# Kernel tuning notes

Measured on AMD Instinct MI355X. Metric: run time of the kernel, lower is better.

Reference implementation:

```python
import jax, jax.numpy as jnp
import numpy as np

B, L, DIM, H, DQK, DV = 4, 512, 1024, 8, 64, 64
ANGLE_BASE = 1.0 / 1024.0
EPS = 1e-5


def _xavier(key, out_d, in_d, gain):
    bound = gain * np.sqrt(6.0 / (in_d + out_d))
    return jax.random.uniform(key, (out_d, in_d), jnp.float32, -bound, bound)


def setup_inputs():
    key = jax.random.key(0)
    ks = jax.random.split(key, 9)
    # p_angle buffer: angle_base ** linspace(0,1,H*DQK) reshaped to [H, DQK]
    p_angle = (ANGLE_BASE ** jnp.linspace(0.0, 1.0, H * DQK)).reshape(H, DQK)
    return {
        "x": jax.random.normal(ks[0], (B, L, DIM), jnp.float32),
        "hidden": 0.1 * jax.random.normal(ks[1], (B, H, DQK, DV, 2), jnp.float32),
        "w_qk": _xavier(ks[2], H * DQK * 4, DIM, 0.01), "b_qk": jnp.zeros((H * DQK * 4,), jnp.float32),
        "w_v": _xavier(ks[3], H * DV * 2, DIM, 0.01), "b_v": jnp.zeros((H * DV * 2,), jnp.float32),
        "w_g": _xavier(ks[4], H * DV * 2, DIM, 0.01), "b_g": jnp.zeros((H * DV * 2,), jnp.float32),
        "w_a": _xavier(ks[5], H, DIM, 1e-4), "b_a": jnp.zeros((H,), jnp.float32),
        "w_y": _xavier(ks[6], DIM, H * DV * 2, 0.01), "b_y": jnp.zeros((DIM,), jnp.float32),
        "gn_w": jnp.ones((H,), jnp.float32), "gn_b": jnp.zeros((H,), jnp.float32),
        "p_angle": p_angle,
    }


def _sioconv(x, hidden, w_qk, b_qk, w_v, b_v, w_g, b_g, w_a, b_a, w_y, b_y, gn_w, gn_b, p_angle):
    b, l = x.shape[0], x.shape[1]
    hid = hidden[..., 0] + 1j * hidden[..., 1]                       # [B,H,I,V] complex
    v_r = (x @ w_v.T + b_v).reshape(b, l, H, DV, 2)
    v = v_r[..., 0] + 1j * v_r[..., 1]                                # [B,L,H,V]
    qk_r = (x @ w_qk.T + b_qk).reshape(b, l, H, DQK, 2, 2)
    qk = qk_r[..., 0] + 1j * qk_r[..., 1]                             # [B,L,H,I,2]
    q, k = qk[..., 0], qk[..., 1]
    a_angle = x @ w_a.T + b_a                                         # [B,L,H]
    ln_a = (1j * a_angle - 1.0) * p_angle[:, 0]                       # [B,L,H] complex
    t = jnp.arange(l, dtype=jnp.float32)
    ppq = jnp.exp(1j * (t[:, None, None] * p_angle[None]))            # [L,H,I] = exp(+i*angle*l)
    qp = q * ppq[None]
    kp = k * jnp.conj(ppq)[None]                                      # exp(-i*angle*l)
    # Decay matrix. The FFT conv with ones computes a causal prefix sum, so
    # c[b,h,l,m] = exp(sum_{j=m+1..l} ln_a[b,j,h]) for m<=l, else 0.
    S = jnp.cumsum(ln_a, axis=1)                                      # [B,L,H]
    Sh = jnp.transpose(S, (0, 2, 1))                                  # [B,H,L]
    mask = jnp.tril(jnp.ones((l, l), bool))
    diff = jnp.where(mask, Sh[:, :, :, None] - Sh[:, :, None, :], 0.0)
    c = jnp.where(mask, jnp.exp(diff), 0.0)                           # [B,H,L,L]
    qck = jnp.einsum('blhi,bmhi->bhlm', qp, kp) * c
    h_inner = jnp.einsum('bhlm,bmhv->blhv', qck, v)
    d = jnp.exp(S)                                                    # [B,L,H] cumulative decay
    p1 = jnp.exp(1j * p_angle)                                        # [H,I]
    h_cross = jnp.einsum('blhi,bhiv->blhv', qp * d[..., None], hid * p1[None, :, :, None])
    h = h_inner + h_cross                                             # [B,L,H,V]
    pp_inv = jnp.exp(1j * ((l - 1.0 - t)[:, None, None] * p_angle[None]))  # [L,H,I]
    hid_next = jnp.einsum('blhi,bhl,lhi,blhv->bhiv', k, c[:, :, -1, :], pp_inv, v)
    hid_next = hid_next + jnp.exp(S[:, -1, :])[:, :, None, None] * hid * jnp.exp(1j * p_angle * l)[None, :, :, None]
    # GroupNorm(num_head, num_head) on real view [B*L, H, V, 2]: normalize over (V,2) per head.
    hr = jnp.stack([h.real, h.imag], axis=-1)                         # [B,L,H,V,2]
    mu = hr.mean(axis=(3, 4), keepdims=True)
    var = hr.var(axis=(3, 4), keepdims=True)
    hn = (hr - mu) / jnp.sqrt(var + EPS)
    hn = hn * gn_w[None, None, :, None, None] + gn_b[None, None, :, None, None]
    h_flat = hn.reshape(b, l, H * DV * 2)
    g = x @ w_g.T + b_g
    y = (h_flat * (g * jax.nn.sigmoid(g))) @ w_y.T + b_y
    return y, hid_next


def reference(x, hidden, w_qk, b_qk, w_v, b_v, w_g, b_g, w_a, b_a, w_y, b_y, gn_w, gn_b, p_angle):
    return _sioconv(x, hidden, w_qk, b_qk, w_v, b_v, w_g, b_g, w_a, b_a, w_y, b_y, gn_w, gn_b, p_angle)
```

## Files before the change

kernel.cpp:

```cpp
#include <hip/hip_runtime.h>
#include <cstdint>
#include <cstddef>

#define B_   4
#define L_   512
#define DIM_ 1024
#define H_   8
#define DQK_ 64
#define DV_  64
#define M_   (B_ * L_)
#define EPS_ 1e-5f

typedef __attribute__((ext_vector_type(8))) short short8;
typedef __attribute__((ext_vector_type(4))) float f32x4;

__device__ __forceinline__ unsigned short f2bf(float f) {
    uint32_t u = __float_as_uint(f);
    u += 0x7FFFu + ((u >> 16) & 1u);
    return (unsigned short)(u >> 16);
}
__device__ __forceinline__ float bf2f(unsigned short u) {
    return __uint_as_float((uint32_t)u << 16);
}

__device__ __forceinline__ f32x4 mm16(short8 a, short8 b, f32x4 c) {
    return __builtin_amdgcn_mfma_f32_16x16x32_bf16(a, b, c, 0, 0, 0);
}

__device__ __forceinline__ int swoff(int r, int kb) {
    return r * 128 + (kb ^ ((r & 7) << 4));
}
__device__ __forceinline__ short8 frag(const unsigned short* p, int strip, int ks, int lane) {
    const int fr = lane & 15, fq = lane >> 4;
    const int r = strip * 16 + fr;
    return *(const short8*)((const char*)p + swoff(r, ks * 64 + fq * 16));
}

__global__ __launch_bounds__(256) void cast_all(
    const float* __restrict__ x, const float* __restrict__ wqk,
    const float* __restrict__ wv, const float* __restrict__ wg,
    const float* __restrict__ wy, const float* __restrict__ wa,
    const float* __restrict__ ba,
    unsigned short* __restrict__ xb, unsigned short* __restrict__ wall,
    unsigned short* __restrict__ wyb, float* __restrict__ babias)
{
    const int blk = blockIdx.x;
    if (blk == 7176) {
        if (threadIdx.x < 128)
            babias[threadIdx.x] = (threadIdx.x < 8) ? ba[threadIdx.x] : 0.f;
        return;
    }
    const float* src; unsigned short* dst; int base;
    if      (blk < 2048) { src = x;   dst = xb;                  base = blk; }
    else if (blk < 4096) { src = wqk; dst = wall;                base = blk - 2048; }
    else if (blk < 5120) { src = wv;  dst = wall + 2048 * 1024;  base = blk - 4096; }
    else if (blk < 6144) { src = wg;  dst = wall + 3072 * 1024;  base = blk - 5120; }
    else if (blk < 7168) { src = wy;  dst = wyb;                 base = blk - 6144; }
    else                 { src = wa;  dst = wall + 4096 * 1024;  base = blk - 7168; }
    const int i = base * 256 + threadIdx.x;
    const float4 v = ((const float4*)src)[i];
    ushort4 o;
    o.x = f2bf(v.x); o.y = f2bf(v.y); o.z = f2bf(v.z); o.w = f2bf(v.w);
    ((ushort4*)dst)[i] = o;
}

__device__ __forceinline__ void gload16(const void* g, void* l) {
    __builtin_amdgcn_global_load_lds(
        (const __attribute__((address_space(1))) unsigned int*)g,
        (__attribute__((address_space(3))) unsigned int*)l, 16, 0, 0);
}

__global__ __launch_bounds__(512) void gemm_proj(
    const unsigned short* __restrict__ A, const unsigned short* __restrict__ W,
    const float* __restrict__ bias0, const float* __restrict__ bias1,
    const float* __restrict__ bias2, const float* __restrict__ bias3,
    void* __restrict__ C0, void* __restrict__ C1,
    void* __restrict__ C2, void* __restrict__ C3,
    int n1, int n2, int n3,
    int ld0, int ld1, int ld2, int ld3,
    int bf0, int bf1, int bf2, int bf3,
    int M, int N, int K)
{
    __shared__ unsigned short sA[128 * 32];
    __shared__ unsigned short sB[128 * 32];

    const int t    = threadIdx.x;
    const int lane = t & 63;
    const int wv   = t >> 6;
    const int bm   = blockIdx.y * 128;
    const int bn   = blockIdx.x * 128;
    const int wr   = wv >> 2;
    const int wc   = wv & 3;
    const int fr   = lane & 15;
    const int fq   = lane >> 4;
    const int srow = lane >> 2;
    const int ske  = (lane & 3) * 8;

    f32x4 acc[4][2] = {};

    for (int k0 = 0; k0 < K; k0 += 32) {
        gload16(A + (size_t)(bm + wv * 16 + srow) * K + k0 + ske,
                (char*)sA + wv * 1024);
        gload16(W + (size_t)(bn + wv * 16 + srow) * K + k0 + ske,
                (char*)sB + wv * 1024);
        __syncthreads();

        short8 af[4], bf[2];
#pragma unroll
        for (int mi = 0; mi < 4; ++mi)
            af[mi] = *(const short8*)&sA[(wr * 64 + mi * 16 + fr) * 32 + fq * 8];
#pragma unroll
        for (int ni = 0; ni < 2; ++ni)
            bf[ni] = *(const short8*)&sB[(wc * 32 + ni * 16 + fr) * 32 + fq * 8];
#pragma unroll
        for (int mi = 0; mi < 4; ++mi)
#pragma unroll
            for (int ni = 0; ni < 2; ++ni)
                acc[mi][ni] = mm16(af[mi], bf[ni], acc[mi][ni]);
        __syncthreads();
    }

    void* Cb; const float* bb; int coff, ldc, isbf;
    if      (bn < n1) { Cb = C0; bb = bias0; coff = 0;  ldc = ld0; isbf = bf0; }
    else if (bn < n2) { Cb = C1; bb = bias1; coff = n1; ldc = ld1; isbf = bf1; }
    else if (bn < n3) { Cb = C2; bb = bias2; coff = n2; ldc = ld2; isbf = bf2; }
    else              { Cb = C3; bb = bias3; coff = n3; ldc = ld3; isbf = bf3; }

#pragma unroll
    for (int mi = 0; mi < 4; ++mi)
#pragma unroll
        for (int ni = 0; ni < 2; ++ni) {
            const int col = bn + wc * 32 + ni * 16 + fr - coff;
            const float bv = bb[col];
#pragma unroll
            for (int r = 0; r < 4; ++r) {
                const int row = bm + wr * 64 + mi * 16 + fq * 4 + r;
                const float val = acc[mi][ni][r] + bv;
                if (isbf)
                    ((unsigned short*)Cb)[(size_t)row * ldc + col] = f2bf(val);
                else
                    ((float*)Cb)[(size_t)row * ldc + col] = val;
            }
        }
}

__global__ __launch_bounds__(256) void gemm_y(
    const unsigned short* __restrict__ A, const unsigned short* __restrict__ W,
    const float* __restrict__ bias, float* __restrict__ C,
    int M, int N, int K)
{
    __shared__ unsigned short sA[64 * 32];
    __shared__ unsigned short sB[64 * 32];

    const int t    = threadIdx.x;
    const int lane = t & 63;
    const int wv   = t >> 6;
    const int bm   = blockIdx.y * 64;
    const int bn   = blockIdx.x * 64;
    const int wr   = wv >> 1;
    const int wc   = wv & 1;
    const int fr   = lane & 15;
    const int fq   = lane >> 4;
    const int srow = lane >> 2;
    const int ske  = (lane & 3) * 8;

    f32x4 acc[2][2] = {};

    for (int k0 = 0; k0 < K; k0 += 32) {
        gload16(A + (size_t)(bm + wv * 16 + srow) * K + k0 + ske,
                (char*)sA + wv * 1024);
        gload16(W + (size_t)(bn + wv * 16 + srow) * K + k0 + ske,
                (char*)sB + wv * 1024);
        __syncthreads();

        short8 af[2], bf[2];
#pragma unroll
        for (int mi = 0; mi < 2; ++mi)
            af[mi] = *(const short8*)&sA[(wr * 32 + mi * 16 + fr) * 32 + fq * 8];
#pragma unroll
        for (int ni = 0; ni < 2; ++ni)
            bf[ni] = *(const short8*)&sB[(wc * 32 + ni * 16 + fr) * 32 + fq * 8];
#pragma unroll
        for (int mi = 0; mi < 2; ++mi)
#pragma unroll
            for (int ni = 0; ni < 2; ++ni)
                acc[mi][ni] = mm16(af[mi], bf[ni], acc[mi][ni]);
        __syncthreads();
    }

#pragma unroll
    for (int mi = 0; mi < 2; ++mi)
#pragma unroll
        for (int ni = 0; ni < 2; ++ni) {
            const int col = bn + wc * 32 + ni * 16 + fr;
            const float bv = bias[col];
#pragma unroll
            for (int r = 0; r < 4; ++r) {
                const int row = bm + wr * 32 + mi * 16 + fq * 4 + r;
                C[(size_t)row * N + col] = acc[mi][ni][r] + bv;
            }
        }
}

__global__ __launch_bounds__(256) void chunkA_mfma(
    const unsigned short* __restrict__ qk_bf, const unsigned short* __restrict__ v_bf,
    const float* __restrict__ a_pad, const float* __restrict__ p_angle,
    float* __restrict__ h_pre, float* __restrict__ Zloc,
    float* __restrict__ Gbuf, float* __restrict__ Wbuf)
{
    const int blk = blockIdx.x;
    const int c  = blk & 7;
    const int bh = blk >> 3;
    const int b = bh >> 3, h = bh & 7;
    const int t = threadIdx.x;
    const int l0 = c * 64;

    __shared__ unsigned short pQr[4096], pQi[4096];
    __shared__ unsigned short pKr[4096], pKi[4096];
    __shared__ unsigned short pKtr[4096], pKti[4096];
    __shared__ unsigned short pVtr[4096], pVti[4096];
    __shared__ float sW[64][4];
    __shared__ float sTh[64];

    if (t < 64) {
        sTh[t] = p_angle[h * DQK_ + t];
        const float th0 = p_angle[h * DQK_];
        const float a = a_pad[((size_t)(b * L_) + l0 + t) * 128 + h];
        float sa, ca; __sincosf(a * th0, &sa, &ca);
        const float em = expf(-th0), ep = expf(th0);
        float lr = em * ca, li = em * sa;
        float ir = ep * ca, ii = -ep * sa;
#pragma unroll
        for (int off = 1; off < 64; off <<= 1) {
            const float plr = __shfl_up(lr, off);
            const float pli = __shfl_up(li, off);
            const float pir = __shfl_up(ir, off);
            const float pii = __shfl_up(ii, off);
            if (t >= off) {
                float nr = lr * plr - li * pli;
                float ni = lr * pli + li * plr;
                lr = nr; li = ni;
                nr = ir * pir - ii * pii;
                ni = ir * pii + ii * pir;
                ir = nr; ii = ni;
            }
        }
        sW[t][0] = lr; sW[t][1] = li; sW[t][2] = ir; sW[t][3] = ii;
        Wbuf[((size_t)bh * L_ + l0 + t) * 2 + 0] = lr;
        Wbuf[((size_t)bh * L_ + l0 + t) * 2 + 1] = li;
        if (t == 63) {
            Gbuf[(bh * 8 + c) * 2 + 0] = lr;
            Gbuf[(bh * 8 + c) * 2 + 1] = li;
        }
    }
    __syncthreads();

    const int row = t >> 2, cs = t & 3;
    {
        const float wr = sW[row][0], wi = sW[row][1];
        const float xr = sW[row][2], xi = sW[row][3];
        const float lf = (float)(l0 + row);
        unsigned short qr16[16], qi16[16], kr16[16], ki16[16];
        const unsigned short* qg = qk_bf +
            (size_t)(b * L_ + l0 + row) * 2048 + h * 256 + cs * 64;
#pragma unroll
        for (int j = 0; j < 16; ++j) {
            const ushort4 qu = *(const ushort4*)(qg + j * 4);
            const float qre = bf2f(qu.x), qim = bf2f(qu.y);
            const float kre = bf2f(qu.z), kim = bf2f(qu.w);
            float sn, cn; __sincosf(sTh[cs * 16 + j] * lf, &sn, &cn);
            const float fqr = cn * wr - sn * wi, fqi = cn * wi + sn * wr;
            const float fkr = cn * xr + sn * xi, fki = cn * xi - sn * xr;
            qr16[j] = f2bf(qre * fqr - qim * fqi);
            qi16[j] = f2bf(qre * fqi + qim * fqr);
            const float kr = kre * fkr - kim * fki;
            const float ki = kre * fki + kim * fkr;
            kr16[j] = f2bf(kr); ki16[j] = f2bf(ki);
            const int i = cs * 16 + j;
            const int ob = swoff(i, 2 * row);
            *(unsigned short*)((char*)pKtr + ob) = kr16[j];
            *(unsigned short*)((char*)pKti + ob) = ki16[j];
        }
        const int kb0 = 32 * cs;
        short8 s0, s1;
#pragma unroll
        for (int j = 0; j < 8; ++j) { s0[j] = (short)qr16[j]; s1[j] = (short)qr16[8 + j]; }
        *(short8*)((char*)pQr + swoff(row, kb0))      = s0;
        *(short8*)((char*)pQr + swoff(row, kb0 + 16)) = s1;
#pragma unroll
        for (int j = 0; j < 8; ++j) { s0[j] = (short)qi16[j]; s1[j] = (short)qi16[8 + j]; }
        *(short8*)((char*)pQi + swoff(row, kb0))      = s0;
        *(short8*)((char*)pQi + swoff(row, kb0 + 16)) = s1;
#pragma unroll
        for (int j = 0; j < 8; ++j) { s0[j] = (short)kr16[j]; s1[j] = (short)kr16[8 + j]; }
        *(short8*)((char*)pKr + swoff(row, kb0))      = s0;
        *(short8*)((char*)pKr + swoff(row, kb0 + 16)) = s1;
#pragma unroll
        for (int j = 0; j < 8; ++j) { s0[j] = (short)ki16[j]; s1[j] = (short)ki16[8 + j]; }
        *(short8*)((char*)pKi + swoff(row, kb0))      = s0;
        *(short8*)((char*)pKi + swoff(row, kb0 + 16)) = s1;

        const unsigned short* vg = v_bf +
            (size_t)(b * L_ + l0 + row) * 1024 + h * 128 + cs * 32;
#pragma unroll
        for (int j = 0; j < 16; ++j) {
            const ushort2 vv = *(const ushort2*)(vg + j * 2);
            const int v = cs * 16 + j;
            const int ob = swoff(v, 2 * row);
            *(unsigned short*)((char*)pVtr + ob) = vv.x;
            *(unsigned short*)((char*)pVti + ob) = vv.y;
        }
    }
    __syncthreads();

    const int w = t >> 6, lane = t & 63;
    const int fr = lane & 15, fq = lane >> 4;
    short8 aQr0 = frag(pQr, w, 0, lane), aQr1 = frag(pQr, w, 1, lane);
    short8 aQi0 = frag(pQi, w, 0, lane), aQi1 = frag(pQi, w, 1, lane);
    f32x4 Pr[4], Pi[4];
#pragma unroll
    for (int tm = 0; tm < 4; ++tm) {
        short8 bKr0 = frag(pKr, tm, 0, lane), bKr1 = frag(pKr, tm, 1, lane);
        short8 bKi0 = frag(pKi, tm, 0, lane), bKi1 = frag(pKi, tm, 1, lane);
        f32x4 tmp = {};
        tmp = mm16(aQi0, bKi0, tmp); tmp = mm16(aQi1, bKi1, tmp);
        tmp = -tmp;
        tmp = mm16(aQr0, bKr0, tmp); tmp = mm16(aQr1, bKr1, tmp);
        Pr[tm] = tmp;
        f32x4 t2 = {};
        t2 = mm16(aQr0, bKi0, t2); t2 = mm16(aQr1, bKi1, t2);
        t2 = mm16(aQi0, bKr0, t2); t2 = mm16(aQi1, bKr1, t2);
        Pi[tm] = t2;
    }
#pragma unroll
    for (int tm = 0; tm < 4; ++tm) {
        const int m = tm * 16 + fr;
#pragma unroll
        for (int r = 0; r < 4; ++r) {
            const int l = w * 16 + fq * 4 + r;
            const int ob = swoff(l, 2 * m);
            const float prv = (m <= l) ? Pr[tm][r] : 0.f;
            const float piv = (m <= l) ? Pi[tm][r] : 0.f;
            *(unsigned short*)((char*)pQr + ob) = f2bf(prv);
            *(unsigned short*)((char*)pQi + ob) = f2bf(piv);
        }
    }

    short8 aPr0 = frag(pQr, w, 0, lane), aPr1 = frag(pQr, w, 1, lane);
    short8 aPi0 = frag(pQi, w, 0, lane), aPi1 = frag(pQi, w, 1, lane);
    short8 aKt_r0 = frag(pKtr, w, 0, lane), aKt_r1 = frag(pKtr, w, 1, lane);
    short8 aKt_i0 = frag(pKti, w, 0, lane), aKt_i1 = frag(pKti, w, 1, lane);
    const float Gr = sW[63][0], Gi = sW[63][1];
#pragma unroll
    for (int tv = 0; tv < 4; ++tv) {
        short8 bVr0 = frag(pVtr, tv, 0, lane), bVr1 = frag(pVtr, tv, 1, lane);
        short8 bVi0 = frag(pVti, tv, 0, lane), bVi1 = frag(pVti, tv, 1, lane);
        f32x4 hr = {};
        hr = mm16(aPi0, bVi0, hr); hr = mm16(aPi1, bVi1, hr);
        hr = -hr;
        hr = mm16(aPr0, bVr0, hr); hr = mm16(aPr1, bVr1, hr);
        f32x4 hi = {};
        hi = mm16(aPr0, bVi0, hi); hi = mm16(aPr1, bVi1, hi);
        hi = mm16(aPi0, bVr0, hi); hi = mm16(aPi1, bVr1, hi);
        f32x4 zr = {};
        zr = mm16(aKt_i0, bVi0, zr); zr = mm16(aKt_i1, bVi1, zr);
        zr = -zr;
        zr = mm16(aKt_r0, bVr0, zr); zr = mm16(aKt_r1, bVr1, zr);
        f32x4 zi = {};
        zi = mm16(aKt_r0, bVi0, zi); zi = mm16(aKt_r1, bVi1, zi);
        zi = mm16(aKt_i0, bVr0, zi); zi = mm16(aKt_i1, bVr1, zi);
#pragma unroll
        for (int r = 0; r < 4; ++r) {
            const int lrow = w * 16 + fq * 4 + r;
            const int v = tv * 16 + fr;
            *(float2*)(h_pre + (((size_t)(b * L_ + l0 + lrow) * H_ + h) * 64 + v) * 2)
                = make_float2(hr[r], hi[r]);
            float* zp = Zloc + (((size_t)(bh * 8 + c) * 4096) + lrow * 64 + v) * 2;
            zp[0] = Gr * zr[r] - Gi * zi[r];
            zp[1] = Gr * zi[r] + Gi * zr[r];
        }
    }
}

__global__ __launch_bounds__(512) void scanB(
    float* __restrict__ Zbuf, const float* __restrict__ Gbuf,
    const float* __restrict__ hidden, const float* __restrict__ p_angle,
    float* __restrict__ hid_out, int real_only)
{
    const int bid = blockIdx.x;
    const int bh = bid >> 3, part = bid & 7;
    const int h = bh & 7;
    const int e = part * 512 + threadIdx.x;
    const int i = e >> 6;
    const float th = p_angle[h * 64 + i];
    float s, c; __sincosf(th, &s, &c);
    const float2 h0 = *(const float2*)(hidden + ((size_t)bh * 4096 + e) * 2);
    float zr = h0.x * c - h0.y * s;
    float zi = h0.x * s + h0.y * c;
#pragma unroll
    for (int ch = 0; ch < 8; ++ch) {
        float* zp = Zbuf + ((size_t)(bh * 8 + ch) * 4096 + e) * 2;
        const float zlr = zp[0], zli = zp[1];
        zp[0] = zr; zp[1] = zi;
        const float gr = Gbuf[(bh * 8 + ch) * 2], gi = Gbuf[(bh * 8 + ch) * 2 + 1];
        const float nr = gr * zr - gi * zi + zlr;
        const float ni = gr * zi + gi * zr + zli;
        zr = nr; zi = ni;
    }
    float s2, c2; __sincosf(th * (float)(L_ - 1), &s2, &c2);
    const float outr = zr * c2 - zi * s2;
    const float outi = zr * s2 + zi * c2;
    if (real_only) {
        hid_out[(size_t)bh * 4096 + e] = outr;
    } else {
        hid_out[((size_t)bh * 4096 + e) * 2 + 0] = outr;
        hid_out[((size_t)bh * 4096 + e) * 2 + 1] = outi;
    }
}

__global__ __launch_bounds__(256) void chunkC_gn(
    const unsigned short* __restrict__ qk_bf, const float* __restrict__ Wbuf,
    const float* __restrict__ Zin, const float* __restrict__ p_angle,
    const float* __restrict__ h_intra, const float* __restrict__ gbuf,
    const float* __restrict__ gn_w, const float* __restrict__ gn_b,
    unsigned short* __restrict__ act)
{
    const int blk = blockIdx.x;
    const int c = blk & 7, bh = blk >> 3;
    const int b = bh >> 3, h = bh & 7;
    const int t = threadIdx.x;
    const int l0 = c * 64;

    __shared__ unsigned short pQr[4096], pQi[4096];
    __shared__ unsigned short pZtr[4096], pZti[4096];
    __shared__ float sTh[64];

    if (t < 64) sTh[t] = p_angle[h * 64 + t];
    __syncthreads();

    const int row = t >> 2, cs = t & 3;
    {
        const float wr = Wbuf[((size_t)bh * L_ + l0 + row) * 2];
        const float wi = Wbuf[((size_t)bh * L_ + l0 + row) * 2 + 1];
        const float lf = (float)(l0 + row);
        unsigned short qr16[16], qi16[16];
        const unsigned short* qg = qk_bf +
            (size_t)(b * L_ + l0 + row) * 2048 + h * 256 + cs * 64;
#pragma unroll
        for (int j = 0; j < 16; ++j) {
            const ushort4 qu = *(const ushort4*)(qg + j * 4);
            const float qre = bf2f(qu.x), qim = bf2f(qu.y);
            float sn, cn; __sincosf(sTh[cs * 16 + j] * lf, &sn, &cn);
            const float fqr = cn * wr - sn * wi, fqi = cn * wi + sn * wr;
            qr16[j] = f2bf(qre * fqr - qim * fqi);
            qi16[j] = f2bf(qre * fqi + qim * fqr);
        }
        const int kb0 = 32 * cs;
        short8 s0, s1;
#pragma unroll
        for (int j = 0; j < 8; ++j) { s0[j] = (short)qr16[j]; s1[j] = (short)qr16[8 + j]; }
        *(short8*)((char*)pQr + swoff(row, kb0))      = s0;
        *(short8*)((char*)pQr + swoff(row, kb0 + 16)) = s1;
#pragma unroll
        for (int j = 0; j < 8; ++j) { s0[j] = (short)qi16[j]; s1[j] = (short)qi16[8 + j]; }
        *(short8*)((char*)pQi + swoff(row, kb0))      = s0;
        *(short8*)((char*)pQi + swoff(row, kb0 + 16)) = s1;

        const float2* zg = (const float2*)(Zin +
            ((size_t)(bh * 8 + c) * 4096 + row * 64 + cs * 16) * 2);
#pragma unroll
        for (int j = 0; j < 16; ++j) {
            const float2 z = zg[j];
            const int v = cs * 16 + j;
            const int ob = swoff(v, 2 * row);
            *(unsigned short*)((char*)pZtr + ob) = f2bf(z.x);
            *(unsigned short*)((char*)pZti + ob) = f2bf(z.y);
        }
    }
    __syncthreads();

    const int w = t >> 6, lane = t & 63;
    const int fr = lane & 15, fq = lane >> 4;
    short8 aQr0 = frag(pQr, w, 0, lane), aQr1 = frag(pQr, w, 1, lane);
    short8 aQi0 = frag(pQi, w, 0, lane), aQi1 = frag(pQi, w, 1, lane);

    float hreg[4][4][2];
#pragma unroll
    for (int tv = 0; tv < 4; ++tv) {
        short8 bZr0 = frag(pZtr, tv, 0, lane), bZr1 = frag(pZtr, tv, 1, lane);
        short8 bZi0 = frag(pZti, tv, 0, lane), bZi1 = frag(pZti, tv, 1, lane);
        f32x4 hr = {};
        hr = mm16(aQi0, bZi0, hr); hr = mm16(aQi1, bZi1, hr);
        hr = -hr;
        hr = mm16(aQr0, bZr0, hr); hr = mm16(aQr1, bZr1, hr);
        f32x4 hi = {};
        hi = mm16(aQr0, bZi0, hi); hi = mm16(aQr1, bZi1, hi);
        hi = mm16(aQi0, bZr0, hi); hi = mm16(aQi1, bZr1, hi);
#pragma unroll
        for (int r = 0; r < 4; ++r) {
            const int l = w * 16 + fq * 4 + r;
            const int v = tv * 16 + fr;
            const float2 hin = *(const float2*)(h_intra +
                (((size_t)(b * L_ + l0 + l) * H_ + h) * 64 + v) * 2);
            hreg[tv][r][0] = hin.x + hr[r];
            hreg[tv][r][1] = hin.y + hi[r];
        }
    }

    const float gw = gn_w[h], gbn = gn_b[h];
    float mean4[4], scl4[4];
#pragma unroll
    for (int r = 0; r < 4; ++r) {
        float s = 0.f, q = 0.f;
#pragma unroll
        for (int tv = 0; tv < 4; ++tv) {
            s += hreg[tv][r][0] + hreg[tv][r][1];
            q += hreg[tv][r][0] * hreg[tv][r][0] + hreg[tv][r][1] * hreg[tv][r][1];
        }
#pragma unroll
        for (int off = 1; off < 16; off <<= 1) {
            s += __shfl_xor(s, off);
            q += __shfl_xor(q, off);
        }
        const float m = s * (1.f / 128.f);
        const float var = q * (1.f / 128.f) - m * m;
        mean4[r] = m;
        scl4[r] = rsqrtf(var + EPS_) * gw;
    }

#pragma unroll
    for (int tv = 0; tv < 4; ++tv) {
#pragma unroll
        for (int r = 0; r < 4; ++r) {
            const int l = w * 16 + fq * 4 + r;
            const int v = tv * 16 + fr;
            const size_t base = (size_t)(b * L_ + l0 + l) * 1024 + h * 128 + v * 2;
            const float2 gv = *(const float2*)(gbuf + base);
            const float hn0 = (hreg[tv][r][0] - mean4[r]) * scl4[r] + gbn;
            const float hn1 = (hreg[tv][r][1] - mean4[r]) * scl4[r] + gbn;
            const float a0 = hn0 * gv.x / (1.f + expf(-gv.x));
            const float a1 = hn1 * gv.y / (1.f + expf(-gv.y));
            ushort2 o; o.x = f2bf(a0); o.y = f2bf(a1);
            *(ushort2*)(act + base) = o;
        }
    }
}

extern "C" void kernel_launch(void* const* d_in, const int* in_sizes, int n_in,
                              void* d_out, int out_size, void* d_ws, size_t ws_size,
                              hipStream_t stream)
{
    (void)in_sizes; (void)n_in; (void)ws_size;
    const float* x       = (const float*)d_in[0];
    const float* hidden  = (const float*)d_in[1];
    const float* w_qk    = (const float*)d_in[2];
    const float* b_qk    = (const float*)d_in[3];
    const float* w_v     = (const float*)d_in[4];
    const float* b_v     = (const float*)d_in[5];
    const float* w_g     = (const float*)d_in[6];
    const float* b_g     = (const float*)d_in[7];
    const float* w_a     = (const float*)d_in[8];
    const float* b_a     = (const float*)d_in[9];
    const float* w_y     = (const float*)d_in[10];
    const float* b_y     = (const float*)d_in[11];
    const float* gn_w    = (const float*)d_in[12];
    const float* gn_b    = (const float*)d_in[13];
    const float* p_angle = (const float*)d_in[14];

    float* y_out   = (float*)d_out;
    float* hid_out = (float*)d_out + (size_t)M_ * DIM_;
    const int hid_elems = out_size - M_ * DIM_;
    const int real_only = (hid_elems == B_ * H_ * DQK_ * DV_) ? 1 : 0;

    unsigned short* xb     = (unsigned short*)d_ws;
    unsigned short* wall   = xb   + (size_t)2048 * 1024;
    unsigned short* wyb    = wall + (size_t)4224 * 1024;
    unsigned short* bqk    = wyb  + (size_t)1024 * 1024;
    unsigned short* bv     = bqk  + (size_t)2048 * 2048;
    unsigned short* actb   = bv   + (size_t)2048 * 1024;
    float* bg     = (float*)(actb + (size_t)2048 * 1024);
    float* ba_pad = bg     + (size_t)2048 * 1024;
    float* babias = ba_pad + (size_t)2048 * 128;
    float* bufW   = babias + 128;
    float* bufG   = bufW   + 32 * 512 * 2;
    float* bufZ   = bufG   + 512;
    float* bufh   = bufZ   + (size_t)32 * 8 * 4096 * 2;

    cast_all<<<7177, 256, 0, stream>>>(x, w_qk, w_v, w_g, w_y, w_a, b_a,
                                       xb, wall, wyb, babias);

    gemm_proj<<<dim3(33, 16), 512, 0, stream>>>(
        xb, wall, b_qk, b_v, b_g, babias,
        bqk, bv, bg, ba_pad,
        2048, 3072, 4096,
        2048, 1024, 1024, 128,
        1, 1, 0, 0,
        M_, 4224, DIM_);

    chunkA_mfma<<<B_*H_*8, 256, 0, stream>>>(
        bqk, bv, ba_pad, p_angle, bufh, bufZ, bufG, bufW);
    scanB<<<B_*H_*8, 512, 0, stream>>>(
        bufZ, bufG, hidden, p_angle, hid_out, real_only);
    chunkC_gn<<<B_*H_*8, 256, 0, stream>>>(
        bqk, bufW, bufZ, p_angle, bufh, bg, gn_w, gn_b, actb);

    gemm_y<<<dim3(16, 32), 256, 0, stream>>>(
        actb, wyb, b_y, y_out, M_, DIM_, DIM_);
}
```

Before: 89.79 us.

## Fuse chunk, scan and GroupNorm kernels into one cooperative kernel with grid sync

Merges the three per-chunk kernels (intra-chunk attention, inter-chunk state scan, inter-chunk correction plus GroupNorm) into a single cooperative launch that uses grid.sync between phases. The intra-chunk h and the rotated Q stay in registers and shared memory instead of round-tripping through the h_pre and Wbuf global buffers. Each block now recomputes the prefix state for its own chunk by walking over all earlier chunks' Zloc, which replaces the separate scan kernel with redundant serial work. This removes two kernel launches and global traffic, at the cost of a grid-wide barrier, extra shared memory, and a serial scan whose length grows with chunk index.

```diff
diff --git a/kernel.cpp b/kernel.cpp
--- a/kernel.cpp
+++ b/kernel.cpp
@@ -1,6 +1,9 @@
 #include <hip/hip_runtime.h>
+#include <hip/hip_cooperative_groups.h>
 #include <cstdint>
 #include <cstddef>
+
+namespace cg = cooperative_groups;
 
 #define B_   4
 #define L_   512
@@ -202,12 +205,22 @@
         }
 }
 
-__global__ __launch_bounds__(256) void chunkA_mfma(
-    const unsigned short* __restrict__ qk_bf, const unsigned short* __restrict__ v_bf,
-    const float* __restrict__ a_pad, const float* __restrict__ p_angle,
-    float* __restrict__ h_pre, float* __restrict__ Zloc,
-    float* __restrict__ Gbuf, float* __restrict__ Wbuf)
+__global__ __launch_bounds__(256) void fused_chunks(
+    const unsigned short* __restrict__ qk_bf,
+    const unsigned short* __restrict__ v_bf,
+    const float* __restrict__ a_pad,
+    const float* __restrict__ p_angle,
+    const float* __restrict__ hidden,
+    const float* __restrict__ gbuf,
+    const float* __restrict__ gn_w,
+    const float* __restrict__ gn_b,
+    float* __restrict__ Zloc,
+    float* __restrict__ Gbuf,
+    unsigned short* __restrict__ act,
+    float* __restrict__ hid_out,
+    int real_only)
 {
+    cg::grid_group grid = cg::this_grid();
     const int blk = blockIdx.x;
     const int c  = blk & 7;
     const int bh = blk >> 3;
@@ -219,8 +232,10 @@
     __shared__ unsigned short pKr[4096], pKi[4096];
     __shared__ unsigned short pKtr[4096], pKti[4096];
     __shared__ unsigned short pVtr[4096], pVti[4096];
+    __shared__ unsigned short pPr[4096], pPi[4096];
     __shared__ float sW[64][4];
     __shared__ float sTh[64];
+    __shared__ float sG[8][2];
 
     if (t < 64) {
         sTh[t] = p_angle[h * DQK_ + t];
@@ -246,8 +261,6 @@
             }
         }
         sW[t][0] = lr; sW[t][1] = li; sW[t][2] = ir; sW[t][3] = ii;
-        Wbuf[((size_t)bh * L_ + l0 + t) * 2 + 0] = lr;
-        Wbuf[((size_t)bh * L_ + l0 + t) * 2 + 1] = li;
         if (t == 63) {
             Gbuf[(bh * 8 + c) * 2 + 0] = lr;
             Gbuf[(bh * 8 + c) * 2 + 1] = li;
@@ -315,180 +328,129 @@
 
     const int w = t >> 6, lane = t & 63;
     const int fr = lane & 15, fq = lane >> 4;
-    short8 aQr0 = frag(pQr, w, 0, lane), aQr1 = frag(pQr, w, 1, lane);
-    short8 aQi0 = frag(pQi, w, 0, lane), aQi1 = frag(pQi, w, 1, lane);
-    f32x4 Pr[4], Pi[4];
-#pragma unroll
-    for (int tm = 0; tm < 4; ++tm) {
-        short8 bKr0 = frag(pKr, tm, 0, lane), bKr1 = frag(pKr, tm, 1, lane);
-        short8 bKi0 = frag(pKi, tm, 0, lane), bKi1 = frag(pKi, tm, 1, lane);
-        f32x4 tmp = {};
-        tmp = mm16(aQi0, bKi0, tmp); tmp = mm16(aQi1, bKi1, tmp);
-        tmp = -tmp;
-        tmp = mm16(aQr0, bKr0, tmp); tmp = mm16(aQr1, bKr1, tmp);
-        Pr[tm] = tmp;
-        f32x4 t2 = {};
-        t2 = mm16(aQr0, bKi0, t2); t2 = mm16(aQr1, bKi1, t2);
-        t2 = mm16(aQi0, bKr0, t2); t2 = mm16(aQi1, bKr1, t2);
-        Pi[tm] = t2;
-    }
-#pragma unroll
-    for (int tm = 0; tm < 4; ++tm) {
-        const int m = tm * 16 + fr;
-#pragma unroll
-        for (int r = 0; r < 4; ++r) {
-            const int l = w * 16 + fq * 4 + r;
-            const int ob = swoff(l, 2 * m);
-            const float prv = (m <= l) ? Pr[tm][r] : 0.f;
-            const float piv = (m <= l) ? Pi[tm][r] : 0.f;
-            *(unsigned short*)((char*)pQr + ob) = f2bf(prv);
-            *(unsigned short*)((char*)pQi + ob) = f2bf(piv);
-        }
-    }
-
-    short8 aPr0 = frag(pQr, w, 0, lane), aPr1 = frag(pQr, w, 1, lane);
-    short8 aPi0 = frag(pQi, w, 0, lane), aPi1 = frag(pQi, w, 1, lane);
-    short8 aKt_r0 = frag(pKtr, w, 0, lane), aKt_r1 = frag(pKtr, w, 1, lane);
-    short8 aKt_i0 = frag(pKti, w, 0, lane), aKt_i1 = frag(pKti, w, 1, lane);
-    const float Gr = sW[63][0], Gi = sW[63][1];
+    {
+        short8 aQr0 = frag(pQr, w, 0, lane), aQr1 = frag(pQr, w, 1, lane);
+        short8 aQi0 = frag(pQi, w, 0, lane), aQi1 = frag(pQi, w, 1, lane);
+        f32x4 Pr[4], Pi[4];
+#pragma unroll
+        for (int tm = 0; tm < 4; ++tm) {
+            short8 bKr0 = frag(pKr, tm, 0, lane), bKr1 = frag(pKr, tm, 1, lane);
+            short8 bKi0 = frag(pKi, tm, 0, lane), bKi1 = frag(pKi, tm, 1, lane);
+            f32x4 tmp = {};
+            tmp = mm16(aQi0, bKi0, tmp); tmp = mm16(aQi1, bKi1, tmp);
+            tmp = -tmp;
+            tmp = mm16(aQr0, bKr0, tmp); tmp = mm16(aQr1, bKr1, tmp);
+            Pr[tm] = tmp;
+            f32x4 t2 = {};
+            t2 = mm16(aQr0, bKi0, t2); t2 = mm16(aQr1, bKi1, t2);
+            t2 = mm16(aQi0, bKr0, t2); t2 = mm16(aQi1, bKr1, t2);
+            Pi[tm] = t2;
+        }
+#pragma unroll
+        for (int tm = 0; tm < 4; ++tm) {
+            const int m = tm * 16 + fr;
+#pragma unroll
+            for (int r = 0; r < 4; ++r) {
+                const int l = w * 16 + fq * 4 + r;
+                const int ob = swoff(l, 2 * m);
+                const float prv = (m <= l) ? Pr[tm][r] : 0.f;
+                const float piv = (m <= l) ? Pi[tm][r] : 0.f;
+                *(unsigned short*)((char*)pPr + ob) = f2bf(prv);
+                *(unsigned short*)((char*)pPi + ob) = f2bf(piv);
+            }
+        }
+    }
+
+    float hreg[4][4][2];
+    {
+        short8 aPr0 = frag(pPr, w, 0, lane), aPr1 = frag(pPr, w, 1, lane);
+        short8 aPi0 = frag(pPi, w, 0, lane), aPi1 = frag(pPi, w, 1, lane);
+        short8 aKt_r0 = frag(pKtr, w, 0, lane), aKt_r1 = frag(pKtr, w, 1, lane);
+        short8 aKt_i0 = frag(pKti, w, 0, lane), aKt_i1 = frag(pKti, w, 1, lane);
+        const float Gr = sW[63][0], Gi = sW[63][1];
+#pragma unroll
+        for (int tv = 0; tv < 4; ++tv) {
+            short8 bVr0 = frag(pVtr, tv, 0, lane), bVr1 = frag(pVtr, tv, 1, lane);
+            short8 bVi0 = frag(pVti, tv, 0, lane), bVi1 = frag(pVti, tv, 1, lane);
+            f32x4 hr = {};
+            hr = mm16(aPi0, bVi0, hr); hr = mm16(aPi1, bVi1, hr);
+            hr = -hr;
+            hr = mm16(aPr0, bVr0, hr); hr = mm16(aPr1, bVr1, hr);
+            f32x4 hi = {};
+            hi = mm16(aPr0, bVi0, hi); hi = mm16(aPr1, bVi1, hi);
+            hi = mm16(aPi0, bVr0, hi); hi = mm16(aPi1, bVr1, hi);
+            f32x4 zr = {};
+            zr = mm16(aKt_i0, bVi0, zr); zr = mm16(aKt_i1, bVi1, zr);
+            zr = -zr;
+            zr = mm16(aKt_r0, bVr0, zr); zr = mm16(aKt_r1, bVr1, zr);
+            f32x4 zi = {};
+            zi = mm16(aKt_r0, bVi0, zi); zi = mm16(aKt_r1, bVi1, zi);
+            zi = mm16(aKt_i0, bVr0, zi); zi = mm16(aKt_i1, bVr1, zi);
+#pragma unroll
+            for (int r = 0; r < 4; ++r) {
+                const int lrow = w * 16 + fq * 4 + r;
+                const int v = tv * 16 + fr;
+                hreg[tv][r][0] = hr[r];
+                hreg[tv][r][1] = hi[r];
+                float* zp = Zloc + (((size_t)(bh * 8 + c) * 4096) + lrow * 64 + v) * 2;
+                zp[0] = Gr * zr[r] - Gi * zi[r];
+                zp[1] = Gr * zi[r] + Gi * zr[r];
+            }
+        }
+    }
+
+    __threadfence();
+    grid.sync();
+
+    if (t < 8) {
+        sG[t][0] = Gbuf[(bh * 8 + t) * 2 + 0];
+        sG[t][1] = Gbuf[(bh * 8 + t) * 2 + 1];
+    }
+    __syncthreads();
+
+#pragma unroll
+    for (int k = 0; k < 16; ++k) {
+        const int e = k * 256 + t;
+        const int i = e >> 6, v = e & 63;
+        const float th = sTh[i];
+        float sn, cn; __sincosf(th, &sn, &cn);
+        const float2 h0 = *(const float2*)(hidden + ((size_t)bh * 4096 + e) * 2);
+        float zr = h0.x * cn - h0.y * sn;
+        float zi = h0.x * sn + h0.y * cn;
+        for (int j = 0; j < c; ++j) {
+            const float gr = sG[j][0], gi = sG[j][1];
+            const float2 zl = *(const float2*)(Zloc + ((size_t)(bh * 8 + j) * 4096 + e) * 2);
+            const float nr = gr * zr - gi * zi + zl.x;
+            const float ni = gr * zi + gi * zr + zl.y;
+            zr = nr; zi = ni;
+        }
+        const int ob = swoff(v, 2 * i);
+        *(unsigned short*)((char*)pKr + ob) = f2bf(zr);
+        *(unsigned short*)((char*)pKi + ob) = f2bf(zi);
+        if (c == 7) {
+            const float gr = sG[7][0], gi = sG[7][1];
+            const float2 zl = *(const float2*)(Zloc + ((size_t)(bh * 8 + 7) * 4096 + e) * 2);
+            const float fr2 = gr * zr - gi * zi + zl.x;
+            const float fi2 = gr * zi + gi * zr + zl.y;
+            float s2, c2v; __sincosf(th * (float)(L_ - 1), &s2, &c2v);
+            const float outr = fr2 * c2v - fi2 * s2;
+            const float outi = fr2 * s2 + fi2 * c2v;
+            if (real_only) {
+                hid_out[(size_t)bh * 4096 + e] = outr;
+            } else {
+                hid_out[((size_t)bh * 4096 + e) * 2 + 0] = outr;
+                hid_out[((size_t)bh * 4096 + e) * 2 + 1] = outi;
+            }
+        }
+    }
+    __syncthreads();
+
 #pragma unroll
     for (int tv = 0; tv < 4; ++tv) {
-        short8 bVr0 = frag(pVtr, tv, 0, lane), bVr1 = frag(pVtr, tv, 1, lane);
-        short8 bVi0 = frag(pVti, tv, 0, lane), bVi1 = frag(pVti, tv, 1, lane);
-        f32x4 hr = {};
-        hr = mm16(aPi0, bVi0, hr); hr = mm16(aPi1, bVi1, hr);
-        hr = -hr;
-        hr = mm16(aPr0, bVr0, hr); hr = mm16(aPr1, bVr1, hr);
-        f32x4 hi = {};
-        hi = mm16(aPr0, bVi0, hi); hi = mm16(aPr1, bVi1, hi);
-        hi = mm16(aPi0, bVr0, hi); hi = mm16(aPi1, bVr1, hi);
-        f32x4 zr = {};
-        zr = mm16(aKt_i0, bVi0, zr); zr = mm16(aKt_i1, bVi1, zr);
-        zr = -zr;
-        zr = mm16(aKt_r0, bVr0, zr); zr = mm16(aKt_r1, bVr1, zr);
-        f32x4 zi = {};
-        zi = mm16(aKt_r0, bVi0, zi); zi = mm16(aKt_r1, bVi1, zi);
-        zi = mm16(aKt_i0, bVr0, zi); zi = mm16(aKt_i1, bVr1, zi);
-#pragma unroll
-        for (int r = 0; r < 4; ++r) {
-            const int lrow = w * 16 + fq * 4 + r;
-            const int v = tv * 16 + fr;
-            *(float2*)(h_pre + (((size_t)(b * L_ + l0 + lrow) * H_ + h) * 64 + v) * 2)
-                = make_float2(hr[r], hi[r]);
-            float* zp = Zloc + (((size_t)(bh * 8 + c) * 4096) + lrow * 64 + v) * 2;
-            zp[0] = Gr * zr[r] - Gi * zi[r];
-            zp[1] = Gr * zi[r] + Gi * zr[r];
-        }
-    }
-}
-
-__global__ __launch_bounds__(512) void scanB(
-    float* __restrict__ Zbuf, const float* __restrict__ Gbuf,
-    const float* __restrict__ hidden, const float* __restrict__ p_angle,
-    float* __restrict__ hid_out, int real_only)
-{
-    const int bid = blockIdx.x;
-    const int bh = bid >> 3, part = bid & 7;
-    const int h = bh & 7;
-    const int e = part * 512 + threadIdx.x;
-    const int i = e >> 6;
-    const float th = p_angle[h * 64 + i];
-    float s, c; __sincosf(th, &s, &c);
-    const float2 h0 = *(const float2*)(hidden + ((size_t)bh * 4096 + e) * 2);
-    float zr = h0.x * c - h0.y * s;
-    float zi = h0.x * s + h0.y * c;
-#pragma unroll
-    for (int ch = 0; ch < 8; ++ch) {
-        float* zp = Zbuf + ((size_t)(bh * 8 + ch) * 4096 + e) * 2;
-        const float zlr = zp[0], zli = zp[1];
-        zp[0] = zr; zp[1] = zi;
-        const float gr = Gbuf[(bh * 8 + ch) * 2], gi = Gbuf[(bh * 8 + ch) * 2 + 1];
-        const float nr = gr * zr - gi * zi + zlr;
-        const float ni = gr * zi + gi * zr + zli;
-        zr = nr; zi = ni;
-    }
-    float s2, c2; __sincosf(th * (float)(L_ - 1), &s2, &c2);
-    const float outr = zr * c2 - zi * s2;
-    const float outi = zr * s2 + zi * c2;
-    if (real_only) {
-        hid_out[(size_t)bh * 4096 + e] = outr;
-    } else {
-        hid_out[((size_t)bh * 4096 + e) * 2 + 0] = outr;
-        hid_out[((size_t)bh * 4096 + e) * 2 + 1] = outi;
-    }
-}
-
-__global__ __launch_bounds__(256) void chunkC_gn(
-    const unsigned short* __restrict__ qk_bf, const float* __restrict__ Wbuf,
-    const float* __restrict__ Zin, const float* __restrict__ p_angle,
-    const float* __restrict__ h_intra, const float* __restrict__ gbuf,
-    const float* __restrict__ gn_w, const float* __restrict__ gn_b,
-    unsigned short* __restrict__ act)
-{
-    const int blk = blockIdx.x;
-    const int c = blk & 7, bh = blk >> 3;
-    const int b = bh >> 3, h = bh & 7;
-    const int t = threadIdx.x;
-    const int l0 = c * 64;
-
-    __shared__ unsigned short pQr[4096], pQi[4096];
-    __shared__ unsigned short pZtr[4096], pZti[4096];
-    __shared__ float sTh[64];
-
-    if (t < 64) sTh[t] = p_angle[h * 64 + t];
-    __syncthreads();
-
-    const int row = t >> 2, cs = t & 3;
-    {
-        const float wr = Wbuf[((size_t)bh * L_ + l0 + row) * 2];
-        const float wi = Wbuf[((size_t)bh * L_ + l0 + row) * 2 + 1];
-        const float lf = (float)(l0 + row);
-        unsigned short qr16[16], qi16[16];
-        const unsigned short* qg = qk_bf +
-            (size_t)(b * L_ + l0 + row) * 2048 + h * 256 + cs * 64;
-#pragma unroll
-        for (int j = 0; j < 16; ++j) {
-            const ushort4 qu = *(const ushort4*)(qg + j * 4);
-            const float qre = bf2f(qu.x), qim = bf2f(qu.y);
-            float sn, cn; __sincosf(sTh[cs * 16 + j] * lf, &sn, &cn);
-            const float fqr = cn * wr - sn * wi, fqi = cn * wi + sn * wr;
-            qr16[j] = f2bf(qre * fqr - qim * fqi);
-            qi16[j] = f2bf(qre * fqi + qim * fqr);
-        }
-        const int kb0 = 32 * cs;
-        short8 s0, s1;
-#pragma unroll
-        for (int j = 0; j < 8; ++j) { s0[j] = (short)qr16[j]; s1[j] = (short)qr16[8 + j]; }
-        *(short8*)((char*)pQr + swoff(row, kb0))      = s0;
-        *(short8*)((char*)pQr + swoff(row, kb0 + 16)) = s1;
-#pragma unroll
-        for (int j = 0; j < 8; ++j) { s0[j] = (short)qi16[j]; s1[j] = (short)qi16[8 + j]; }
-        *(short8*)((char*)pQi + swoff(row, kb0))      = s0;
-        *(short8*)((char*)pQi + swoff(row, kb0 + 16)) = s1;
-
-        const float2* zg = (const float2*)(Zin +
-            ((size_t)(bh * 8 + c) * 4096 + row * 64 + cs * 16) * 2);
-#pragma unroll
-        for (int j = 0; j < 16; ++j) {
-            const float2 z = zg[j];
-            const int v = cs * 16 + j;
-            const int ob = swoff(v, 2 * row);
-            *(unsigned short*)((char*)pZtr + ob) = f2bf(z.x);
-            *(unsigned short*)((char*)pZti + ob) = f2bf(z.y);
-        }
-    }
-    __syncthreads();
-
-    const int w = t >> 6, lane = t & 63;
-    const int fr = lane & 15, fq = lane >> 4;
-    short8 aQr0 = frag(pQr, w, 0, lane), aQr1 = frag(pQr, w, 1, lane);
-    short8 aQi0 = frag(pQi, w, 0, lane), aQi1 = frag(pQi, w, 1, lane);
-
-    float hreg[4][4][2];
-#pragma unroll
-    for (int tv = 0; tv < 4; ++tv) {
-        short8 bZr0 = frag(pZtr, tv, 0, lane), bZr1 = frag(pZtr, tv, 1, lane);
-        short8 bZi0 = frag(pZti, tv, 0, lane), bZi1 = frag(pZti, tv, 1, lane);
+        short8 aQr0 = frag(pQr, w, 0, lane), aQr1 = frag(pQr, w, 1, lane);
+        short8 aQi0 = frag(pQi, w, 0, lane), aQi1 = frag(pQi, w, 1, lane);
+        short8 bZr0 = frag(pKr, tv, 0, lane), bZr1 = frag(pKr, tv, 1, lane);
+        short8 bZi0 = frag(pKi, tv, 0, lane), bZi1 = frag(pKi, tv, 1, lane);
         f32x4 hr = {};
         hr = mm16(aQi0, bZi0, hr); hr = mm16(aQi1, bZi1, hr);
         hr = -hr;
@@ -498,12 +460,8 @@
         hi = mm16(aQi0, bZr0, hi); hi = mm16(aQi1, bZr1, hi);
 #pragma unroll
         for (int r = 0; r < 4; ++r) {
-            const int l = w * 16 + fq * 4 + r;
-            const int v = tv * 16 + fr;
-            const float2 hin = *(const float2*)(h_intra +
-                (((size_t)(b * L_ + l0 + l) * H_ + h) * 64 + v) * 2);
-            hreg[tv][r][0] = hin.x + hr[r];
-            hreg[tv][r][1] = hin.y + hi[r];
+            hreg[tv][r][0] += hr[r];
+            hreg[tv][r][1] += hi[r];
         }
     }
 
@@ -570,7 +528,7 @@
     float* y_out   = (float*)d_out;
     float* hid_out = (float*)d_out + (size_t)M_ * DIM_;
     const int hid_elems = out_size - M_ * DIM_;
-    const int real_only = (hid_elems == B_ * H_ * DQK_ * DV_) ? 1 : 0;
+    int real_only = (hid_elems == B_ * H_ * DQK_ * DV_) ? 1 : 0;
 
     unsigned short* xb     = (unsigned short*)d_ws;
     unsigned short* wall   = xb   + (size_t)2048 * 1024;
@@ -581,10 +539,8 @@
     float* bg     = (float*)(actb + (size_t)2048 * 1024);
     float* ba_pad = bg     + (size_t)2048 * 1024;
     float* babias = ba_pad + (size_t)2048 * 128;
-    float* bufW   = babias + 128;
-    float* bufG   = bufW   + 32 * 512 * 2;
+    float* bufG   = babias + 128;
     float* bufZ   = bufG   + 512;
-    float* bufh   = bufZ   + (size_t)32 * 8 * 4096 * 2;
 
     cast_all<<<7177, 256, 0, stream>>>(x, w_qk, w_v, w_g, w_y, w_a, b_a,
                                        xb, wall, wyb, babias);
@@ -597,12 +553,24 @@
         1, 1, 0, 0,
         M_, 4224, DIM_);
 
-    chunkA_mfma<<<B_*H_*8, 256, 0, stream>>>(
-        bqk, bv, ba_pad, p_angle, bufh, bufZ, bufG, bufW);
-    scanB<<<B_*H_*8, 512, 0, stream>>>(
-        bufZ, bufG, hidden, p_angle, hid_out, real_only);
-    chunkC_gn<<<B_*H_*8, 256, 0, stream>>>(
-        bqk, bufW, bufZ, p_angle, bufh, bg, gn_w, gn_b, actb);
+    {
+        const unsigned short* a0 = bqk;
+        const unsigned short* a1 = bv;
+        const float* a2 = ba_pad;
+        const float* a3 = p_angle;
+        const float* a4 = hidden;
+        const float* a5 = bg;
+        const float* a6 = gn_w;
+        const float* a7 = gn_b;
+        float* a8 = bufZ;
+        float* a9 = bufG;
+        unsigned short* a10 = actb;
+        float* a11 = hid_out;
+        void* args[] = { &a0, &a1, &a2, &a3, &a4, &a5, &a6, &a7,
+                         &a8, &a9, &a10, &a11, &real_only };
+        hipLaunchCooperativeKernel((void*)fused_chunks, dim3(B_ * H_ * 8),
+                                   dim3(256), args, 0, stream);
+    }
 
     gemm_y<<<dim3(16, 32), 256, 0, stream>>>(
         actb, wyb, b_y, y_out, M_, DIM_, DIM_);
```

Measured after the change: 189.8 us. 111% more time.
